# Performance work log

Measured on AMD Instinct MI355X. Metric: run time of the kernel, lower is better.

Reference implementation:

```python
import jax, jax.numpy as jnp
import numpy as np

N, E, C, D, H = 50000, 1600000, 50000, 128, 512


def setup_inputs() -> dict:
    key = jax.random.key(0)
    ks = jax.random.split(key, 16)
    s = jnp.float32(0.02)  # keep activations stable through 3 layers
    inp = {}
    inp["x"] = jax.random.normal(ks[0], (N, D), jnp.float32)
    inp["edge_index"] = jax.random.randint(ks[1], (2, E), 0, N)
    inp["first_edge"] = jax.random.randint(ks[2], (2,), 0, N)
    inp["candidate_edges"] = jax.random.randint(ks[3], (C, 2), 0, N)
    inp["t"] = jax.random.uniform(ks[4], (1, 1), jnp.float32)
    dims = [(D, H), (H, H), (H, H)]
    i = 5
    for l, (di, do) in enumerate(dims):
        inp[f"gin{l}_w1"] = jax.random.normal(ks[i], (di, do), jnp.float32) * s; i += 1
        inp[f"gin{l}_b1"] = jnp.zeros((do,), jnp.float32)
        inp[f"gin{l}_w2"] = jax.random.normal(ks[i], (do, do), jnp.float32) * s; i += 1
        inp[f"gin{l}_b2"] = jnp.zeros((do,), jnp.float32)
    inp["pred_w1"] = jax.random.normal(ks[i], (5 * H, H), jnp.float32) * s; i += 1
    inp["pred_b1"] = jnp.zeros((H,), jnp.float32)
    inp["pred_w2"] = jax.random.normal(ks[i], (H, 1), jnp.float32) * s; i += 1
    inp["pred_b2"] = jnp.zeros((1,), jnp.float32)
    inp["time_w1"] = jax.random.normal(ks[i], (1, H), jnp.float32) * s; i += 1
    inp["time_b1"] = jnp.zeros((H,), jnp.float32)
    inp["time_w2"] = jax.random.normal(ks[i], (H, H), jnp.float32) * s; i += 1
    inp["time_b2"] = jnp.zeros((H,), jnp.float32)
    return inp


def _edge_rep(x, u, v):
    # 'sum_absdiff': cat([x_u + x_v, |x_u - x_v|]) -> 2*H features
    xu, xv = x[u], x[v]
    return jnp.concatenate([xu + xv, jnp.abs(xu - xv)], axis=-1)


def reference(x, edge_index, first_edge, candidate_edges, t,
              gin0_w1, gin0_b1, gin0_w2, gin0_b2,
              gin1_w1, gin1_b1, gin1_w2, gin1_b2,
              gin2_w1, gin2_b1, gin2_w2, gin2_b2,
              pred_w1, pred_b1, pred_w2, pred_b2,
              time_w1, time_b1, time_w2, time_b2):
    src, dst = edge_index[0], edge_index[1]
    layers = [(gin0_w1, gin0_b1, gin0_w2, gin0_b2),
              (gin1_w1, gin1_b1, gin1_w2, gin1_b2),
              (gin2_w1, gin2_b1, gin2_w2, gin2_b2)]
    # GINConv (eps=0): h_i = MLP(x_i + sum_{j->i} x_j)
    for w1, b1, w2, b2 in layers:
        agg = jax.ops.segment_sum(x[src], dst, num_segments=x.shape[0])
        h = x + agg
        x = jax.nn.relu(h @ w1 + b1) @ w2 + b2
    first_feat = _edge_rep(x, first_edge[0], first_edge[1])  # [2H]
    t_embed = (jax.nn.relu(t @ time_w1 + time_b1) @ time_w2 + time_b2)[0]  # [H]
    cand_feat = _edge_rep(x, candidate_edges[:, 0], candidate_edges[:, 1])  # [C, 2H]
    Cn = cand_feat.shape[0]
    feat = jnp.concatenate([
        jnp.broadcast_to(first_feat, (Cn, first_feat.shape[0])),
        cand_feat,
        jnp.broadcast_to(t_embed, (Cn, t_embed.shape[0])),
    ], axis=-1)  # [C, 5H]
    logits = (jax.nn.relu(feat @ pred_w1 + pred_b1) @ pred_w2 + pred_b2)[:, 0]  # [C]
    return logits
```

## Files before the change

### kernel.cpp

```cpp
#include <hip/hip_runtime.h>

typedef __bf16 bf16x2 __attribute__((ext_vector_type(2)));
typedef __bf16 bf16x4 __attribute__((ext_vector_type(4)));
typedef __bf16 bf16x8 __attribute__((ext_vector_type(8)));
typedef float f32x4 __attribute__((ext_vector_type(4)));

#define LDSTR 40
#define CSR_CHUNKS 256

__global__ __launch_bounds__(256)
void hist_part_kernel(const int* __restrict__ dst, int* __restrict__ deg, int E, int N) {
    const int r = blockIdx.x & 7;
    const int chunk = blockIdx.x >> 3;
    const int RS = (N + 7) >> 3;
    const int lo = r * RS;
    const int hi = min(lo + RS, N);
    const int stride = CSR_CHUNKS * 256;
    for (int i = chunk * 256 + threadIdx.x; i < E; i += stride) {
        int d = dst[i];
        if (d >= lo && d < hi) atomicAdd(&deg[d], 1);
    }
}

__global__ __launch_bounds__(256)
void scatter_part_kernel(const int* __restrict__ src, const int* __restrict__ dst,
                         int* __restrict__ cursor, int* __restrict__ colsrc, int E, int N) {
    const int r = blockIdx.x & 7;
    const int chunk = blockIdx.x >> 3;
    const int RS = (N + 7) >> 3;
    const int lo = r * RS;
    const int hi = min(lo + RS, N);
    const int stride = CSR_CHUNKS * 256;
    for (int i = chunk * 256 + threadIdx.x; i < E; i += stride) {
        int d = dst[i];
        if (d >= lo && d < hi) {
            int p = atomicAdd(&cursor[d], 1);
            colsrc[p] = src[i];
        }
    }
}

__global__ __launch_bounds__(256)
void blocksum_kernel(const int* __restrict__ deg, int* __restrict__ bsum, int n) {
    __shared__ int red[256];
    int i = blockIdx.x * 256 + threadIdx.x;
    red[threadIdx.x] = (i < n) ? deg[i] : 0;
    __syncthreads();
    for (int off = 128; off > 0; off >>= 1) {
        if (threadIdx.x < off) red[threadIdx.x] += red[threadIdx.x + off];
        __syncthreads();
    }
    if (threadIdx.x == 0) bsum[blockIdx.x] = red[0];
}

__global__ __launch_bounds__(256)
void scanb_kernel(int* __restrict__ bsum, int nb) {
    __shared__ int s[256];
    int t = threadIdx.x;
    s[t] = (t < nb) ? bsum[t] : 0;
    __syncthreads();
    for (int off = 1; off < 256; off <<= 1) {
        int v = (t >= off) ? s[t - off] : 0;
        __syncthreads();
        s[t] += v;
        __syncthreads();
    }
    if (t < nb) bsum[t] = (t == 0) ? 0 : s[t - 1];
}

__global__ __launch_bounds__(256)
void scanw_kernel(const int* __restrict__ deg, const int* __restrict__ bsum,
                  int* __restrict__ rowptr, int* __restrict__ cursor, int n) {
    __shared__ int s[256];
    int b = blockIdx.x, t = threadIdx.x;
    int i = b * 256 + t;
    int d = (i < n) ? deg[i] : 0;
    s[t] = d;
    __syncthreads();
    for (int off = 1; off < 256; off <<= 1) {
        int v = (t >= off) ? s[t - off] : 0;
        __syncthreads();
        s[t] += v;
        __syncthreads();
    }
    int incl = s[t];
    int base = bsum[b];
    if (i < n) {
        int r = base + incl - d;
        rowptr[i] = r;
        cursor[i] = r;
        if (i == n - 1) rowptr[n] = base + incl;
    }
}

__global__ void f32_to_bf16_kernel(const float* __restrict__ in, __bf16* __restrict__ out, int n4) {
    int i = blockIdx.x * 256 + threadIdx.x;
    if (i < n4) {
        float4 f = ((const float4*)in)[i];
        bf16x4 o;
        o[0] = (__bf16)f.x; o[1] = (__bf16)f.y; o[2] = (__bf16)f.z; o[3] = (__bf16)f.w;
        ((bf16x4*)out)[i] = o;
    }
}

__global__ void wprep_kernel(const float* __restrict__ in, __bf16* __restrict__ out, int kbits) {
    int idx = blockIdx.x * 256 + threadIdx.x;
    int K = 1 << kbits;
    if (idx < (512 << kbits)) {
        int k = idx & (K - 1);
        int n = idx >> kbits;
        out[idx] = (__bf16)in[k * 512 + n];
    }
}

template<int F> struct VecT;
template<> struct VecT<2> { using T = bf16x2; };
template<> struct VecT<4> { using T = bf16x4; };
template<> struct VecT<8> { using T = bf16x8; };

template<int F, int U, int STR>
__global__ __launch_bounds__(256)
void agg_kernel(const __bf16* __restrict__ xb, const int* __restrict__ rowptr,
                const int* __restrict__ colsrc, __bf16* __restrict__ h, int n, int colbase) {
    const int node = blockIdx.x * 4 + (threadIdx.x >> 6);
    if (node >= n) return;
    const int lane = threadIdx.x & 63;
    using V = typename VecT<F>::T;

    const __bf16* xl = xb + colbase + lane * F;

    float acc[F];
    {
        V v = *(const V*)(xl + (size_t)node * STR);
        #pragma unroll
        for (int i = 0; i < F; i++) acc[i] = (float)v[i];
    }

    int e   = __builtin_amdgcn_readfirstlane(rowptr[node]);
    int end = __builtin_amdgcn_readfirstlane(rowptr[node + 1]);

    for (; e + U <= end; e += U) {
        int s[U];
        #pragma unroll
        for (int j = 0; j < U; j++) s[j] = colsrc[e + j];
        V v[U];
        #pragma unroll
        for (int j = 0; j < U; j++) v[j] = *(const V*)(xl + (size_t)s[j] * STR);
        #pragma unroll
        for (int j = 0; j < U; j++)
            #pragma unroll
            for (int i = 0; i < F; i++) acc[i] += (float)v[j][i];
    }
    if constexpr (U > 4) {
        for (; e + 4 <= end; e += 4) {
            int s[4];
            #pragma unroll
            for (int j = 0; j < 4; j++) s[j] = colsrc[e + j];
            V v[4];
            #pragma unroll
            for (int j = 0; j < 4; j++) v[j] = *(const V*)(xl + (size_t)s[j] * STR);
            #pragma unroll
            for (int j = 0; j < 4; j++)
                #pragma unroll
                for (int i = 0; i < F; i++) acc[i] += (float)v[j][i];
        }
    }
    for (; e < end; e++) {
        int s0 = colsrc[e];
        V v = *(const V*)(xl + (size_t)s0 * STR);
        #pragma unroll
        for (int i = 0; i < F; i++) acc[i] += (float)v[i];
    }

    __bf16* out = h + colbase + (size_t)node * STR + lane * F;
    V o;
    #pragma unroll
    for (int i = 0; i < F; i++) o[i] = (__bf16)acc[i];
    *(V*)out = o;
}

template<int AMODE, bool RELU>
__global__ __launch_bounds__(256, 3)
void gemm_kernel(const __bf16* __restrict__ A, const __bf16* __restrict__ Xb,
                 const int* __restrict__ cand, const __bf16* __restrict__ Bt,
                 const float* __restrict__ bias, __bf16* __restrict__ Cout,
                 int M, int K) {
    __shared__ __bf16 sA[2][64 * LDSTR];
    __shared__ __bf16 sB[2][256 * LDSTR];

    const int tid = threadIdx.x;
    const int lane = tid & 63;
    const int waveN = tid >> 6;
    const int mlane = lane & 15;
    const int quad = lane >> 4;
    const int rowBase = blockIdx.x * 64;
    const int nBase = blockIdx.y * 256;

    const int ar = tid >> 2;
    const int ac = (tid & 3) << 3;

    const f32x4 fzero = {0.f, 0.f, 0.f, 0.f};
    f32x4 acc[4][4];
    #pragma unroll
    for (int i = 0; i < 4; i++)
        #pragma unroll
        for (int j = 0; j < 4; j++) acc[i][j] = fzero;

    int uu = 0, vv = 0;
    const int grow = rowBase + ar;
    const bool arowok = (grow < M);
    if (AMODE == 1 && arowok) { uu = cand[2 * grow]; vv = cand[2 * grow + 1]; }

    bf16x8 pa{}, pxu{}, pxv{};
    bf16x8 pb[4];
    int pk = 0;

    auto issue = [&](int k0) {
        pk = k0;
        if (AMODE == 0) {
            pa = {};
            if (arowok) pa = *(const bf16x8*)(A + (size_t)grow * K + k0 + ac);
        } else {
            if (arowok) {
                int kk = (k0 + ac) & 511;
                pxu = *(const bf16x8*)(Xb + (size_t)uu * 512 + kk);
                pxv = *(const bf16x8*)(Xb + (size_t)vv * 512 + kk);
            }
        }
        #pragma unroll
        for (int i = 0; i < 4; i++)
            pb[i] = *(const bf16x8*)(Bt + (size_t)(nBase + ar + i * 64) * K + k0 + ac);
    };

    auto commit = [&](int buf) {
        bf16x8 av;
        if (AMODE == 0) {
            av = pa;
        } else {
            av = bf16x8{};
            if (arowok) {
                if (pk + ac < 512) {
                    #pragma unroll
                    for (int q = 0; q < 8; q++) av[q] = (__bf16)((float)pxu[q] + (float)pxv[q]);
                } else {
                    #pragma unroll
                    for (int q = 0; q < 8; q++) av[q] = (__bf16)fabsf((float)pxu[q] - (float)pxv[q]);
                }
            }
        }
        *(bf16x8*)(sA[buf] + ar * LDSTR + ac) = av;
        #pragma unroll
        for (int i = 0; i < 4; i++)
            *(bf16x8*)(sB[buf] + (ar + i * 64) * LDSTR + ac) = pb[i];
    };

    issue(0);
    commit(0);
    __syncthreads();

    int cur = 0;
    for (int k0 = 0; k0 < K; k0 += 32) {
        const bool more = (k0 + 32 < K);
        if (more) issue(k0 + 32);

        bf16x8 aF[4], bF[4];
        #pragma unroll
        for (int mt = 0; mt < 4; mt++)
            aF[mt] = *(const bf16x8*)(sA[cur] + (mt * 16 + mlane) * LDSTR + quad * 8);
        #pragma unroll
        for (int nt = 0; nt < 4; nt++)
            bF[nt] = *(const bf16x8*)(sB[cur] + (waveN * 64 + nt * 16 + mlane) * LDSTR + quad * 8);
        #pragma unroll
        for (int mt = 0; mt < 4; mt++)
            #pragma unroll
            for (int nt = 0; nt < 4; nt++)
                acc[mt][nt] = __builtin_amdgcn_mfma_f32_16x16x32_bf16(aF[mt], bF[nt], acc[mt][nt], 0, 0, 0);

        if (more) {
            commit(cur ^ 1);
            __syncthreads();
            cur ^= 1;
        }
    }

    #pragma unroll
    for (int mt = 0; mt < 4; mt++) {
        #pragma unroll
        for (int nt = 0; nt < 4; nt++) {
            int col = nBase + waveN * 64 + nt * 16 + mlane;
            float bv = bias[col];
            #pragma unroll
            for (int r = 0; r < 4; r++) {
                int row = rowBase + mt * 16 + quad * 4 + r;
                if (row < M) {
                    float v = acc[mt][nt][r] + bv;
                    if (RELU) v = fmaxf(v, 0.f);
                    Cout[(size_t)row * 512 + col] = (__bf16)v;
                }
            }
        }
    }
}

__global__ __launch_bounds__(512)
void constvec_kernel(const __bf16* __restrict__ xb, const int* __restrict__ first_edge,
                     const float* __restrict__ t,
                     const float* __restrict__ tw1, const float* __restrict__ tb1,
                     const float* __restrict__ tw2, const float* __restrict__ tb2,
                     const float* __restrict__ pw1, const float* __restrict__ pb1,
                     float* __restrict__ cvec) {
    __shared__ float z1[512];
    __shared__ float te[512];
    __shared__ float ff[1024];
    int tid = threadIdx.x;
    float tv = t[0];
    z1[tid] = fmaxf(tv * tw1[tid] + tb1[tid], 0.f);
    int u = first_edge[0], v = first_edge[1];
    float xu = (float)xb[(size_t)u * 512 + tid];
    float xv = (float)xb[(size_t)v * 512 + tid];
    ff[tid] = xu + xv;
    ff[512 + tid] = fabsf(xu - xv);
    __syncthreads();
    float s = tb2[tid];
    for (int j = 0; j < 512; j++) s += z1[j] * tw2[j * 512 + tid];
    te[tid] = s;
    __syncthreads();
    float c = pb1[tid];
    for (int k = 0; k < 1024; k++) c += ff[k] * pw1[k * 512 + tid];
    for (int j = 0; j < 512; j++) c += te[j] * pw1[(2048 + j) * 512 + tid];
    cvec[tid] = c;
}

__global__ __launch_bounds__(256)
void logits_kernel(const __bf16* __restrict__ Z, const float* __restrict__ w2,
                   const float* __restrict__ b2, float* __restrict__ out, int C) {
    int c = blockIdx.x * 4 + (threadIdx.x >> 6);
    if (c >= C) return;
    int lane = threadIdx.x & 63;
    bf16x8 z = *(const bf16x8*)(Z + (size_t)c * 512 + lane * 8);
    const float4* w = (const float4*)(w2 + lane * 8);
    float4 w0 = w[0], w1 = w[1];
    float s = (float)z[0] * w0.x + (float)z[1] * w0.y + (float)z[2] * w0.z + (float)z[3] * w0.w
            + (float)z[4] * w1.x + (float)z[5] * w1.y + (float)z[6] * w1.z + (float)z[7] * w1.w;
    #pragma unroll
    for (int off = 32; off > 0; off >>= 1) s += __shfl_down(s, off);
    if (lane == 0) out[c] = s + b2[0];
}

extern "C" void kernel_launch(void* const* d_in, const int* in_sizes, int n_in,
                              void* d_out, int out_size, void* d_ws, size_t ws_size,
                              hipStream_t stream) {
    (void)n_in; (void)out_size; (void)ws_size;
    const float* x          = (const float*)d_in[0];
    const int*   edge_index = (const int*)d_in[1];
    const int*   first_edge = (const int*)d_in[2];
    const int*   cand       = (const int*)d_in[3];
    const float* t          = (const float*)d_in[4];
    const float* gw1[3] = {(const float*)d_in[5], (const float*)d_in[9],  (const float*)d_in[13]};
    const float* gb1[3] = {(const float*)d_in[6], (const float*)d_in[10], (const float*)d_in[14]};
    const float* gw2[3] = {(const float*)d_in[7], (const float*)d_in[11], (const float*)d_in[15]};
    const float* gb2[3] = {(const float*)d_in[8], (const float*)d_in[12], (const float*)d_in[16]};
    const float* pw1 = (const float*)d_in[17];
    const float* pb1 = (const float*)d_in[18];
    const float* pw2 = (const float*)d_in[19];
    const float* pb2 = (const float*)d_in[20];
    const float* tw1 = (const float*)d_in[21];
    const float* tb1 = (const float*)d_in[22];
    const float* tw2 = (const float*)d_in[23];
    const float* tb2 = (const float*)d_in[24];

    const int N = in_sizes[0] / 128;
    const int E = in_sizes[1] / 2;
    const int C = in_sizes[3] / 2;

    char* p = (char*)d_ws;
    auto alloc = [&](size_t bytes) -> void* {
        void* r = (void*)p;
        p += (bytes + 255) & ~(size_t)255;
        return r;
    };
    __bf16* h    = (__bf16*)alloc((size_t)N * 512 * 2);
    __bf16* u    = (__bf16*)alloc((size_t)N * 512 * 2);
    __bf16* xb   = (__bf16*)alloc((size_t)N * 512 * 2);
    __bf16* wt01 = (__bf16*)alloc((size_t)512 * 128 * 2);
    __bf16* wt02 = (__bf16*)alloc((size_t)512 * 512 * 2);
    __bf16* wt11 = (__bf16*)alloc((size_t)512 * 512 * 2);
    __bf16* wt12 = (__bf16*)alloc((size_t)512 * 512 * 2);
    __bf16* wt21 = (__bf16*)alloc((size_t)512 * 512 * 2);
    __bf16* wt22 = (__bf16*)alloc((size_t)512 * 512 * 2);
    __bf16* wtH  = (__bf16*)alloc((size_t)512 * 1024 * 2);
    int* rowptr = (int*)alloc((size_t)(N + 1) * 4);
    int* deg    = (int*)alloc((size_t)N * 4);
    int* cursor = (int*)alloc((size_t)N * 4);
    int* colsrc = (int*)alloc((size_t)E * 4);
    int* bsum   = (int*)alloc((size_t)256 * 4);
    float* cvec = (float*)alloc(512 * 4);
    __bf16* xb0 = (__bf16*)u;

    const int* src = edge_index;
    const int* dst = edge_index + E;

    hipMemsetAsync(deg, 0, (size_t)N * 4, stream);
    int nb = (N + 255) / 256;
    hist_part_kernel<<<CSR_CHUNKS * 8, 256, 0, stream>>>(dst, deg, E, N);
    blocksum_kernel<<<nb, 256, 0, stream>>>(deg, bsum, N);
    scanb_kernel<<<1, 256, 0, stream>>>(bsum, nb);
    scanw_kernel<<<nb, 256, 0, stream>>>(deg, bsum, rowptr, cursor, N);
    scatter_part_kernel<<<CSR_CHUNKS * 8, 256, 0, stream>>>(src, dst, cursor, colsrc, E, N);

    f32_to_bf16_kernel<<<((N * 128 / 4) + 255) / 256, 256, 0, stream>>>(x, xb0, N * 128 / 4);
    wprep_kernel<<<((512 << 7)  + 255) / 256, 256, 0, stream>>>(gw1[0], wt01, 7);
    wprep_kernel<<<((512 << 9)  + 255) / 256, 256, 0, stream>>>(gw2[0], wt02, 9);
    wprep_kernel<<<((512 << 9)  + 255) / 256, 256, 0, stream>>>(gw1[1], wt11, 9);
    wprep_kernel<<<((512 << 9)  + 255) / 256, 256, 0, stream>>>(gw2[1], wt12, 9);
    wprep_kernel<<<((512 << 9)  + 255) / 256, 256, 0, stream>>>(gw1[2], wt21, 9);
    wprep_kernel<<<((512 << 9)  + 255) / 256, 256, 0, stream>>>(gw2[2], wt22, 9);
    wprep_kernel<<<((512 << 10) + 255) / 256, 256, 0, stream>>>(pw1 + (size_t)1024 * 512, wtH, 10);

    dim3 ggrid((N + 63) / 64, 2);
    int ablocks = (N + 3) / 4;

    agg_kernel<2, 16, 128><<<ablocks, 256, 0, stream>>>(xb0, rowptr, colsrc, h, N, 0);
    gemm_kernel<0, true ><<<ggrid, 256, 0, stream>>>(h, nullptr, nullptr, wt01, gb1[0], u,  N, 128);
    gemm_kernel<0, false><<<ggrid, 256, 0, stream>>>(u, nullptr, nullptr, wt02, gb2[0], xb, N, 512);
    agg_kernel<4, 8, 512><<<ablocks, 256, 0, stream>>>(xb, rowptr, colsrc, h, N, 0);
    agg_kernel<4, 8, 512><<<ablocks, 256, 0, stream>>>(xb, rowptr, colsrc, h, N, 256);
    gemm_kernel<0, true ><<<ggrid, 256, 0, stream>>>(h, nullptr, nullptr, wt11, gb1[1], u,  N, 512);
    gemm_kernel<0, false><<<ggrid, 256, 0, stream>>>(u, nullptr, nullptr, wt12, gb2[1], xb, N, 512);
    agg_kernel<4, 8, 512><<<ablocks, 256, 0, stream>>>(xb, rowptr, colsrc, h, N, 0);
    agg_kernel<4, 8, 512><<<ablocks, 256, 0, stream>>>(xb, rowptr, colsrc, h, N, 256);
    gemm_kernel<0, true ><<<ggrid, 256, 0, stream>>>(h, nullptr, nullptr, wt21, gb1[2], u,  N, 512);
    gemm_kernel<0, false><<<ggrid, 256, 0, stream>>>(u, nullptr, nullptr, wt22, gb2[2], xb, N, 512);

    constvec_kernel<<<1, 512, 0, stream>>>(xb, first_edge, t, tw1, tb1, tw2, tb2, pw1, pb1, cvec);
    dim3 hgrid((C + 63) / 64, 2);
    gemm_kernel<1, true><<<hgrid, 256, 0, stream>>>(nullptr, xb, cand, wtH, cvec, u, C, 1024);
    logits_kernel<<<(C + 3) / 4, 256, 0, stream>>>(u, pw2, pb2, (float*)d_out, C);
}
```

Before: 1.307 ms.

## Enlarge GEMM tile to 128 rows and stage epilogue through LDS for coalesced stores

Each GEMM block now covers 128x256 output instead of 64x256, with each wave computing 8x4 MFMA tiles. This doubles reuse of the B tile per LDS load and halves the number of blocks re-reading weights. The epilogue writes bias-added fp32 results into shared memory, then emits 16-byte coalesced bf16 row stores instead of scattered 2-byte stores. The cost is higher register pressure (launch bounds lowered to 2 blocks per SM), more LDS, and extra barriers in the epilogue.

```diff
diff --git a/kernel.cpp b/kernel.cpp
--- a/kernel.cpp
+++ b/kernel.cpp
@@ -180,78 +180,91 @@
 }
 
 template<int AMODE, bool RELU>
-__global__ __launch_bounds__(256, 3)
+__global__ __launch_bounds__(256, 2)
 void gemm_kernel(const __bf16* __restrict__ A, const __bf16* __restrict__ Xb,
                  const int* __restrict__ cand, const __bf16* __restrict__ Bt,
                  const float* __restrict__ bias, __bf16* __restrict__ Cout,
                  int M, int K) {
-    __shared__ __bf16 sA[2][64 * LDSTR];
+    __shared__ __bf16 sA[2][128 * LDSTR];
     __shared__ __bf16 sB[2][256 * LDSTR];
 
     const int tid = threadIdx.x;
     const int lane = tid & 63;
-    const int waveN = tid >> 6;
+    const int wid = tid >> 6;
     const int mlane = lane & 15;
     const int quad = lane >> 4;
-    const int rowBase = blockIdx.x * 64;
+    const int rowBase = blockIdx.x * 128;
     const int nBase = blockIdx.y * 256;
 
-    const int ar = tid >> 2;
-    const int ac = (tid & 3) << 3;
+    const int arow = tid >> 1;
+    const int ahalf = (tid & 1) << 4;
+    const int brow = tid;
 
     const f32x4 fzero = {0.f, 0.f, 0.f, 0.f};
-    f32x4 acc[4][4];
+    f32x4 acc[8][4];
     #pragma unroll
-    for (int i = 0; i < 4; i++)
+    for (int i = 0; i < 8; i++)
         #pragma unroll
         for (int j = 0; j < 4; j++) acc[i][j] = fzero;
 
     int uu = 0, vv = 0;
-    const int grow = rowBase + ar;
+    const int grow = rowBase + arow;
     const bool arowok = (grow < M);
     if (AMODE == 1 && arowok) { uu = cand[2 * grow]; vv = cand[2 * grow + 1]; }
 
-    bf16x8 pa{}, pxu{}, pxv{};
+    bf16x8 pa0{}, pa1{}, pxu0{}, pxu1{}, pxv0{}, pxv1{};
     bf16x8 pb[4];
     int pk = 0;
 
     auto issue = [&](int k0) {
         pk = k0;
         if (AMODE == 0) {
-            pa = {};
-            if (arowok) pa = *(const bf16x8*)(A + (size_t)grow * K + k0 + ac);
+            pa0 = bf16x8{}; pa1 = bf16x8{};
+            if (arowok) {
+                pa0 = *(const bf16x8*)(A + (size_t)grow * K + k0 + ahalf);
+                pa1 = *(const bf16x8*)(A + (size_t)grow * K + k0 + ahalf + 8);
+            }
         } else {
             if (arowok) {
-                int kk = (k0 + ac) & 511;
-                pxu = *(const bf16x8*)(Xb + (size_t)uu * 512 + kk);
-                pxv = *(const bf16x8*)(Xb + (size_t)vv * 512 + kk);
+                int kk = (k0 + ahalf) & 511;
+                pxu0 = *(const bf16x8*)(Xb + (size_t)uu * 512 + kk);
+                pxu1 = *(const bf16x8*)(Xb + (size_t)uu * 512 + kk + 8);
+                pxv0 = *(const bf16x8*)(Xb + (size_t)vv * 512 + kk);
+                pxv1 = *(const bf16x8*)(Xb + (size_t)vv * 512 + kk + 8);
             }
         }
         #pragma unroll
-        for (int i = 0; i < 4; i++)
-            pb[i] = *(const bf16x8*)(Bt + (size_t)(nBase + ar + i * 64) * K + k0 + ac);
+        for (int c = 0; c < 4; c++)
+            pb[c] = *(const bf16x8*)(Bt + (size_t)(nBase + brow) * K + k0 + c * 8);
     };
 
     auto commit = [&](int buf) {
-        bf16x8 av;
+        bf16x8 av0, av1;
         if (AMODE == 0) {
-            av = pa;
+            av0 = pa0; av1 = pa1;
         } else {
-            av = bf16x8{};
+            av0 = bf16x8{}; av1 = bf16x8{};
             if (arowok) {
-                if (pk + ac < 512) {
+                if (pk + ahalf < 512) {
                     #pragma unroll
-                    for (int q = 0; q < 8; q++) av[q] = (__bf16)((float)pxu[q] + (float)pxv[q]);
+                    for (int q = 0; q < 8; q++) {
+                        av0[q] = (__bf16)((float)pxu0[q] + (float)pxv0[q]);
+                        av1[q] = (__bf16)((float)pxu1[q] + (float)pxv1[q]);
+                    }
                 } else {
                     #pragma unroll
-                    for (int q = 0; q < 8; q++) av[q] = (__bf16)fabsf((float)pxu[q] - (float)pxv[q]);
+                    for (int q = 0; q < 8; q++) {
+                        av0[q] = (__bf16)fabsf((float)pxu0[q] - (float)pxv0[q]);
+                        av1[q] = (__bf16)fabsf((float)pxu1[q] - (float)pxv1[q]);
+                    }
                 }
             }
         }
-        *(bf16x8*)(sA[buf] + ar * LDSTR + ac) = av;
-        #pragma unroll
-        for (int i = 0; i < 4; i++)
-            *(bf16x8*)(sB[buf] + (ar + i * 64) * LDSTR + ac) = pb[i];
+        *(bf16x8*)(sA[buf] + arow * LDSTR + ahalf) = av0;
+        *(bf16x8*)(sA[buf] + arow * LDSTR + ahalf + 8) = av1;
+        #pragma unroll
+        for (int c = 0; c < 4; c++)
+            *(bf16x8*)(sB[buf] + brow * LDSTR + c * 8) = pb[c];
     };
 
     issue(0);
@@ -263,18 +276,17 @@
         const bool more = (k0 + 32 < K);
         if (more) issue(k0 + 32);
 
-        bf16x8 aF[4], bF[4];
-        #pragma unroll
-        for (int mt = 0; mt < 4; mt++)
-            aF[mt] = *(const bf16x8*)(sA[cur] + (mt * 16 + mlane) * LDSTR + quad * 8);
+        bf16x8 bF[4];
         #pragma unroll
         for (int nt = 0; nt < 4; nt++)
-            bF[nt] = *(const bf16x8*)(sB[cur] + (waveN * 64 + nt * 16 + mlane) * LDSTR + quad * 8);
-        #pragma unroll
-        for (int mt = 0; mt < 4; mt++)
+            bF[nt] = *(const bf16x8*)(sB[cur] + (wid * 64 + nt * 16 + mlane) * LDSTR + quad * 8);
+        #pragma unroll
+        for (int mt = 0; mt < 8; mt++) {
+            bf16x8 aF = *(const bf16x8*)(sA[cur] + (mt * 16 + mlane) * LDSTR + quad * 8);
             #pragma unroll
             for (int nt = 0; nt < 4; nt++)
-                acc[mt][nt] = __builtin_amdgcn_mfma_f32_16x16x32_bf16(aF[mt], bF[nt], acc[mt][nt], 0, 0, 0);
+                acc[mt][nt] = __builtin_amdgcn_mfma_f32_16x16x32_bf16(aF, bF[nt], acc[mt][nt], 0, 0, 0);
+        }
 
         if (more) {
             commit(cur ^ 1);
@@ -283,21 +295,41 @@
         }
     }
 
+    float bv[4];
     #pragma unroll
-    for (int mt = 0; mt < 4; mt++) {
+    for (int nt = 0; nt < 4; nt++) bv[nt] = bias[nBase + wid * 64 + nt * 16 + mlane];
+
+    float* tp = (float*)&sA[0][0];
+    const int erow = tid >> 4;
+    const int ecg = tid & 15;
+    #pragma unroll
+    for (int mt = 0; mt < 8; mt++) {
+        __syncthreads();
         #pragma unroll
         for (int nt = 0; nt < 4; nt++) {
-            int col = nBase + waveN * 64 + nt * 16 + mlane;
-            float bv = bias[col];
             #pragma unroll
             for (int r = 0; r < 4; r++) {
-                int row = rowBase + mt * 16 + quad * 4 + r;
-                if (row < M) {
-                    float v = acc[mt][nt][r] + bv;
-                    if (RELU) v = fmaxf(v, 0.f);
-                    Cout[(size_t)row * 512 + col] = (__bf16)v;
-                }
+                float v = acc[mt][nt][r] + bv[nt];
+                if (RELU) v = fmaxf(v, 0.f);
+                tp[(quad * 4 + r) * 264 + wid * 64 + nt * 16 + mlane] = v;
             }
+        }
+        __syncthreads();
+        int gr = rowBase + mt * 16 + erow;
+        if (gr < M) {
+            const float* rp = tp + erow * 264 + ecg * 16;
+            f32x4 a = *(const f32x4*)(rp);
+            f32x4 b = *(const f32x4*)(rp + 4);
+            f32x4 c = *(const f32x4*)(rp + 8);
+            f32x4 d = *(const f32x4*)(rp + 12);
+            bf16x8 o0, o1;
+            #pragma unroll
+            for (int j = 0; j < 4; j++) { o0[j] = (__bf16)a[j]; o0[4 + j] = (__bf16)b[j]; }
+            #pragma unroll
+            for (int j = 0; j < 4; j++) { o1[j] = (__bf16)c[j]; o1[4 + j] = (__bf16)d[j]; }
+            __bf16* op = Cout + (size_t)gr * 512 + nBase + ecg * 16;
+            *(bf16x8*)op = o0;
+            *(bf16x8*)(op + 8) = o1;
         }
     }
 }
@@ -417,7 +449,7 @@
     wprep_kernel<<<((512 << 9)  + 255) / 256, 256, 0, stream>>>(gw2[2], wt22, 9);
     wprep_kernel<<<((512 << 10) + 255) / 256, 256, 0, stream>>>(pw1 + (size_t)1024 * 512, wtH, 10);
 
-    dim3 ggrid((N + 63) / 64, 2);
+    dim3 ggrid((N + 127) / 128, 2);
     int ablocks = (N + 3) / 4;
 
     agg_kernel<2, 16, 128><<<ablocks, 256, 0, stream>>>(xb0, rowptr, colsrc, h, N, 0);
@@ -433,7 +465,7 @@
     gemm_kernel<0, false><<<ggrid, 256, 0, stream>>>(u, nullptr, nullptr, wt22, gb2[2], xb, N, 512);
 
     constvec_kernel<<<1, 512, 0, stream>>>(xb, first_edge, t, tw1, tb1, tw2, tb2, pw1, pb1, cvec);
-    dim3 hgrid((C + 63) / 64, 2);
+    dim3 hgrid((C + 127) / 128, 2);
     gemm_kernel<1, true><<<hgrid, 256, 0, stream>>>(nullptr, xb, cand, wtH, cvec, u, C, 1024);
     logits_kernel<<<(C + 3) / 4, 256, 0, stream>>>(u, pw2, pb2, (float*)d_out, C);
 }
```

Measured after the change: 1.263 ms. -3.3%, faster.

## Stage GEMM epilogue through LDS for vectorized stores and unroll k-loop by two

Applied to the files above, without the earlier changes.

Replaces the scattered per-element bf16 stores in the GEMM epilogue with a staging pass through shared memory, so that each thread writes contiguous 16-element row segments as two 16-byte stores. The main loop is also manually unrolled by two with separate prefetch register sets, which avoids the buffer index toggle and the branch on every step. The cost is extra barriers per M-tile in the epilogue and more register pressure from the two prefetch structs, which could reduce occupancy under launch_bounds(256,3).

```diff
diff --git a/kernel.cpp b/kernel.cpp
--- a/kernel.cpp
+++ b/kernel.cpp
@@ -185,12 +185,15 @@
                  const int* __restrict__ cand, const __bf16* __restrict__ Bt,
                  const float* __restrict__ bias, __bf16* __restrict__ Cout,
                  int M, int K) {
-    __shared__ __bf16 sA[2][64 * LDSTR];
-    __shared__ __bf16 sB[2][256 * LDSTR];
+    __shared__ __bf16 smem[2 * (64 + 256) * LDSTR];
+    __bf16* const sA0 = smem;
+    __bf16* const sA1 = smem + 64 * LDSTR;
+    __bf16* const sB0 = smem + 128 * LDSTR;
+    __bf16* const sB1 = smem + (128 + 256) * LDSTR;
 
     const int tid = threadIdx.x;
     const int lane = tid & 63;
-    const int waveN = tid >> 6;
+    const int wid = tid >> 6;
     const int mlane = lane & 15;
     const int quad = lane >> 4;
     const int rowBase = blockIdx.x * 64;
@@ -211,93 +214,114 @@
     const bool arowok = (grow < M);
     if (AMODE == 1 && arowok) { uu = cand[2 * grow]; vv = cand[2 * grow + 1]; }
 
-    bf16x8 pa{}, pxu{}, pxv{};
-    bf16x8 pb[4];
-    int pk = 0;
-
-    auto issue = [&](int k0) {
-        pk = k0;
+    struct PF { bf16x8 pa, pxu, pxv; bf16x8 pb[4]; int pk; };
+    PF s0, s1;
+
+    auto issue = [&](PF& S, int k0) {
+        S.pk = k0;
         if (AMODE == 0) {
-            pa = {};
-            if (arowok) pa = *(const bf16x8*)(A + (size_t)grow * K + k0 + ac);
+            S.pa = bf16x8{};
+            if (arowok) S.pa = *(const bf16x8*)(A + (size_t)grow * K + k0 + ac);
         } else {
             if (arowok) {
                 int kk = (k0 + ac) & 511;
-                pxu = *(const bf16x8*)(Xb + (size_t)uu * 512 + kk);
-                pxv = *(const bf16x8*)(Xb + (size_t)vv * 512 + kk);
+                S.pxu = *(const bf16x8*)(Xb + (size_t)uu * 512 + kk);
+                S.pxv = *(const bf16x8*)(Xb + (size_t)vv * 512 + kk);
             }
         }
         #pragma unroll
-        for (int i = 0; i < 4; i++)
-            pb[i] = *(const bf16x8*)(Bt + (size_t)(nBase + ar + i * 64) * K + k0 + ac);
+        for (int c = 0; c < 4; c++)
+            S.pb[c] = *(const bf16x8*)(Bt + (size_t)(nBase + ar + c * 64) * K + k0 + ac);
     };
 
-    auto commit = [&](int buf) {
+    auto commit = [&](PF& S, __bf16* bufA, __bf16* bufB) {
         bf16x8 av;
         if (AMODE == 0) {
-            av = pa;
+            av = S.pa;
         } else {
             av = bf16x8{};
             if (arowok) {
-                if (pk + ac < 512) {
+                if (S.pk + ac < 512) {
                     #pragma unroll
-                    for (int q = 0; q < 8; q++) av[q] = (__bf16)((float)pxu[q] + (float)pxv[q]);
+                    for (int q = 0; q < 8; q++) av[q] = (__bf16)((float)S.pxu[q] + (float)S.pxv[q]);
                 } else {
                     #pragma unroll
-                    for (int q = 0; q < 8; q++) av[q] = (__bf16)fabsf((float)pxu[q] - (float)pxv[q]);
+                    for (int q = 0; q < 8; q++) av[q] = (__bf16)fabsf((float)S.pxu[q] - (float)S.pxv[q]);
                 }
             }
         }
-        *(bf16x8*)(sA[buf] + ar * LDSTR + ac) = av;
-        #pragma unroll
-        for (int i = 0; i < 4; i++)
-            *(bf16x8*)(sB[buf] + (ar + i * 64) * LDSTR + ac) = pb[i];
+        *(bf16x8*)(bufA + ar * LDSTR + ac) = av;
+        #pragma unroll
+        for (int c = 0; c < 4; c++)
+            *(bf16x8*)(bufB + (ar + c * 64) * LDSTR + ac) = S.pb[c];
     };
 
-    issue(0);
-    commit(0);
-    __syncthreads();
-
-    int cur = 0;
-    for (int k0 = 0; k0 < K; k0 += 32) {
-        const bool more = (k0 + 32 < K);
-        if (more) issue(k0 + 32);
-
+    auto compute = [&](const __bf16* bufA, const __bf16* bufB) {
         bf16x8 aF[4], bF[4];
         #pragma unroll
         for (int mt = 0; mt < 4; mt++)
-            aF[mt] = *(const bf16x8*)(sA[cur] + (mt * 16 + mlane) * LDSTR + quad * 8);
+            aF[mt] = *(const bf16x8*)(bufA + (mt * 16 + mlane) * LDSTR + quad * 8);
         #pragma unroll
         for (int nt = 0; nt < 4; nt++)
-            bF[nt] = *(const bf16x8*)(sB[cur] + (waveN * 64 + nt * 16 + mlane) * LDSTR + quad * 8);
+            bF[nt] = *(const bf16x8*)(bufB + (wid * 64 + nt * 16 + mlane) * LDSTR + quad * 8);
         #pragma unroll
         for (int mt = 0; mt < 4; mt++)
             #pragma unroll
             for (int nt = 0; nt < 4; nt++)
                 acc[mt][nt] = __builtin_amdgcn_mfma_f32_16x16x32_bf16(aF[mt], bF[nt], acc[mt][nt], 0, 0, 0);
-
-        if (more) {
-            commit(cur ^ 1);
-            __syncthreads();
-            cur ^= 1;
-        }
-    }
-
+    };
+
+    issue(s0, 0);
+    commit(s0, sA0, sB0);
+    issue(s1, 32);
+    __syncthreads();
+
+    for (int k0 = 0; k0 < K; k0 += 64) {
+        if (k0 + 64 < K) issue(s0, k0 + 64);
+        compute(sA0, sB0);
+        commit(s1, sA1, sB1);
+        __syncthreads();
+        if (k0 + 96 < K) issue(s1, k0 + 96);
+        compute(sA1, sB1);
+        if (k0 + 64 < K) commit(s0, sA0, sB0);
+        __syncthreads();
+    }
+
+    float bv[4];
+    #pragma unroll
+    for (int nt = 0; nt < 4; nt++) bv[nt] = bias[nBase + wid * 64 + nt * 16 + mlane];
+
+    float* tp = (float*)smem;
+    const int erow = tid >> 4;
+    const int ecg = tid & 15;
     #pragma unroll
     for (int mt = 0; mt < 4; mt++) {
+        __syncthreads();
         #pragma unroll
         for (int nt = 0; nt < 4; nt++) {
-            int col = nBase + waveN * 64 + nt * 16 + mlane;
-            float bv = bias[col];
             #pragma unroll
             for (int r = 0; r < 4; r++) {
-                int row = rowBase + mt * 16 + quad * 4 + r;
-                if (row < M) {
-                    float v = acc[mt][nt][r] + bv;
-                    if (RELU) v = fmaxf(v, 0.f);
-                    Cout[(size_t)row * 512 + col] = (__bf16)v;
-                }
+                float v = acc[mt][nt][r] + bv[nt];
+                if (RELU) v = fmaxf(v, 0.f);
+                tp[(quad * 4 + r) * 264 + wid * 64 + nt * 16 + mlane] = v;
             }
+        }
+        __syncthreads();
+        int gr = rowBase + mt * 16 + erow;
+        if (gr < M) {
+            const float* rp = tp + erow * 264 + ecg * 16;
+            f32x4 a = *(const f32x4*)(rp);
+            f32x4 b = *(const f32x4*)(rp + 4);
+            f32x4 c = *(const f32x4*)(rp + 8);
+            f32x4 d = *(const f32x4*)(rp + 12);
+            bf16x8 o0, o1;
+            #pragma unroll
+            for (int j = 0; j < 4; j++) { o0[j] = (__bf16)a[j]; o0[4 + j] = (__bf16)b[j]; }
+            #pragma unroll
+            for (int j = 0; j < 4; j++) { o1[j] = (__bf16)c[j]; o1[4 + j] = (__bf16)d[j]; }
+            __bf16* op = Cout + (size_t)gr * 512 + nBase + ecg * 16;
+            *(bf16x8*)op = o0;
+            *(bf16x8*)(op + 8) = o1;
         }
     }
 }
```

Result: faster. 1.221 ms (-6.5%).
